# Performance work log

Hardware: AMD Instinct MI355X
Metric: run time of the kernel (lower is better)

The kernel has to match this reference:

```python
import jax, jax.numpy as jnp
import numpy as np

B, N, C, H, W = 4, 8, 256, 64, 64
K = 4          # BANK_SIZE
HID = 256      # HIDDEN_DIM
DT = 1.0
TEMP = 1.0     # RETRIEVAL_TEMPERATURE
NUM_ACTIONS = 5


def setup_inputs() -> dict:
    key = jax.random.key(0)
    ks = jax.random.split(key, 8)
    value = jax.random.normal(ks[0], (B, N, C, H, W), dtype=jnp.float32)
    mask = jax.random.uniform(ks[1], (B, N, H, W), dtype=jnp.float32)
    dict_keys = jax.random.normal(ks[2], (B, N, K, C), dtype=jnp.float32)
    dict_vel = jax.random.normal(ks[3], (B, N, K, C), dtype=jnp.float32) * 0.1
    dict_valid = jnp.ones((B, N, K), dtype=bool)
    din = 3 * C + K
    W1 = jax.random.normal(ks[4], (din, HID), dtype=jnp.float32) * 0.05
    b1 = jnp.zeros((HID,), dtype=jnp.float32)
    W2 = jax.random.normal(ks[5], (HID, NUM_ACTIONS), dtype=jnp.float32) * 0.05
    b2 = jnp.zeros((NUM_ACTIONS,), dtype=jnp.float32)
    gate = jnp.ones((1,), dtype=jnp.float32)
    return {"value": value, "mask": mask, "dict_keys": dict_keys, "dict_vel": dict_vel,
            "dict_valid": dict_valid, "W1": W1, "b1": b1, "W2": W2, "b2": b2, "gate": gate}


def _pool_state(value, mask):
    # masked mean pool over HxW (mask already at value resolution -> no interpolation branch)
    denom = mask.sum((-2, -1))                                           # [B,N]
    pooled = jnp.einsum('bnchw,bnhw->bnc', value, mask) / jnp.maximum(denom, 1e-6)[..., None]
    fallback = value.mean((-2, -1))                                      # [B,N,C]
    return jnp.where((denom > 1e-5)[..., None], pooled, fallback)


def _retrieve(z, keys, valid):
    dist = jnp.sum((z[:, :, None, :] - keys) ** 2, axis=-1)              # [B,N,K]
    logits = jnp.where(valid, -dist / TEMP, -1e30)
    w = jax.nn.softmax(logits, axis=-1)
    has = jnp.any(valid, axis=-1)                                        # [B,N]
    w = jnp.where(has[..., None], w, 0.0)
    nearest = jnp.argmin(jnp.where(valid, dist, jnp.inf), axis=-1)
    return w, nearest, has


def _forward(value, mask, dict_keys, dict_vel, dict_valid, W1, b1, W2, b2, gate):
    z = _pool_state(value, mask)                                         # [B,N,C]
    # first retrieval
    w0, n0, has0 = _retrieve(z, dict_keys, dict_valid)
    # branchless conditional spawn: write z into first free slot where no match
    need = ~has0                                                         # [B,N]
    slot = jnp.argmax(~dict_valid, axis=-1)                              # first invalid slot
    write = need[..., None] & (jnp.arange(K) == slot[..., None])         # [B,N,K]
    keys2 = jnp.where(write[..., None], z[:, :, None, :], dict_keys)
    vel2 = jnp.where(write[..., None], 0.0, dict_vel)
    valid2 = dict_valid | write
    # re-retrieve after (possible) spawn
    w, nearest, has = _retrieve(z, keys2, valid2)
    # ODE-style prediction: z_next = z + dt * sum_k w_k * vel_k
    vel_bar = jnp.einsum('bnk,bnkc->bnc', w, vel2)
    z_next = z + DT * vel_bar
    # Q maintainer: MLP over concat state, masked greedy action
    q_state = jnp.concatenate([z, z_next, z_next - z, w], axis=-1)       # [B,N,3C+K]
    h = jax.nn.relu(q_state @ W1 + b1)
    q = h @ W2 + b2                                                      # [B,N,5]
    bank_full = jnp.all(valid2, axis=-1)                                 # [B,N]
    action_mask = jnp.concatenate(
        [jnp.ones(q.shape[:-1] + (NUM_ACTIONS - 1,), bool), (~bank_full)[..., None]], axis=-1)
    q_values = jnp.where(action_mask, q, -1e9)
    actions = jnp.argmax(q_values, axis=-1)                              # [B,N]
    # Q-gated readout: broadcast delta over HxW
    delta = (z_next - z)[..., None, None]                                # [B,N,C,1,1]
    readout = value + gate[0] * delta
    wc = jnp.clip(w, 1e-8, None)
    entropy = -jnp.sum(wc * jnp.log(wc), axis=-1)                        # [B,N]
    hist = jnp.mean(jax.nn.one_hot(actions, NUM_ACTIONS, dtype=jnp.float32), axis=(0, 1))
    return readout, w, q_values, actions, entropy, hist


def reference(value, mask, dict_keys, dict_vel, dict_valid, W1, b1, W2, b2, gate):
    return _forward(value, mask, dict_keys, dict_vel, dict_valid, W1, b1, W2, b2, gate)
```

## Files before the change

kernel.cpp:

```cpp
#include <hip/hip_runtime.h>
#include <math.h>

#define B_ 4
#define N_ 8
#define C_ 256
#define H_ 64
#define Wd_ 64
#define K_ 4
#define HID_ 256
#define NA_ 5
#define HW_ (H_*Wd_)
#define DIN_ (3*C_+K_)
#define QS_STRIDE 800

#define READOUT_N (B_*N_*C_*HW_)
#define W_OFF    READOUT_N
#define Q_OFF    (W_OFF   + B_*N_*K_)
#define ACT_OFF  (Q_OFF   + B_*N_*NA_)
#define ENT_OFF  (ACT_OFF + B_*N_)
#define HIST_OFF (ENT_OFF + B_*N_)

__global__ __launch_bounds__(256) void pool_kernel(const float* __restrict__ value,
                                                   const float* __restrict__ mask,
                                                   float* __restrict__ z) {
    const int bnc = blockIdx.x;
    const int bn  = bnc >> 8;
    const int tid = threadIdx.x;
    const float4* vp = (const float4*)value + (size_t)bnc * (HW_/4);
    const float4* mp = (const float4*)mask  + (size_t)bn  * (HW_/4);
    float smv = 0.f, sv = 0.f, sm = 0.f;
    #pragma unroll
    for (int i = 0; i < (HW_/4)/256; ++i) {
        float4 v = vp[tid + i*256];
        float4 m = mp[tid + i*256];
        smv += v.x*m.x + v.y*m.y + v.z*m.z + v.w*m.w;
        sv  += v.x + v.y + v.z + v.w;
        sm  += m.x + m.y + m.z + m.w;
    }
    #pragma unroll
    for (int o = 32; o > 0; o >>= 1) {
        smv += __shfl_down(smv, o);
        sv  += __shfl_down(sv, o);
        sm  += __shfl_down(sm, o);
    }
    __shared__ float red[3][4];
    const int lane = tid & 63, wid = tid >> 6;
    if (lane == 0) { red[0][wid] = smv; red[1][wid] = sv; red[2][wid] = sm; }
    __syncthreads();
    if (tid == 0) {
        float t_smv = red[0][0]+red[0][1]+red[0][2]+red[0][3];
        float t_sv  = red[1][0]+red[1][1]+red[1][2]+red[1][3];
        float t_sm  = red[2][0]+red[2][1]+red[2][2]+red[2][3];
        float pooled = t_smv / fmaxf(t_sm, 1e-6f);
        float fb     = t_sv * (1.0f/HW_);
        z[bnc] = (t_sm > 1e-5f) ? pooled : fb;
    }
}

__global__ __launch_bounds__(256) void retrieve_kernel(
    const float* __restrict__ z,    const float* __restrict__ keys,
    const float* __restrict__ vel,  const int*   __restrict__ valid,
    float* __restrict__ qs_ws,      float* __restrict__ delta_ws,
    float* __restrict__ full_ws,    float* __restrict__ out)
{
    const int bn = blockIdx.x, tid = threadIdx.x;
    __shared__ float z_s[C_];
    __shared__ float key2[K_][C_];
    __shared__ float vel2[K_][C_];
    __shared__ float red[K_][4];
    __shared__ float w_s[K_];
    __shared__ int   wr_s[K_];
    __shared__ int   valid2_s[K_];

    z_s[tid] = z[bn*C_ + tid];
    if (tid == 0) {
        int v[K_]; bool anyv = false;
        for (int k = 0; k < K_; ++k) { v[k] = (valid[bn*K_ + k] != 0); anyv = anyv || v[k]; }
        int slot = 0;
        for (int k = K_-1; k >= 0; --k) if (!v[k]) slot = k;
        const bool need = !anyv;
        for (int k = 0; k < K_; ++k) {
            int wr = (need && k == slot) ? 1 : 0;
            wr_s[k] = wr;
            valid2_s[k] = v[k] | wr;
        }
    }
    __syncthreads();
    #pragma unroll
    for (int k = 0; k < K_; ++k) {
        key2[k][tid] = wr_s[k] ? z_s[tid] : keys[((size_t)bn*K_+k)*C_ + tid];
        vel2[k][tid] = wr_s[k] ? 0.f      : vel [((size_t)bn*K_+k)*C_ + tid];
    }
    __syncthreads();
    float part[K_];
    #pragma unroll
    for (int k = 0; k < K_; ++k) { float d = z_s[tid] - key2[k][tid]; part[k] = d*d; }
    #pragma unroll
    for (int o = 32; o > 0; o >>= 1) {
        #pragma unroll
        for (int k = 0; k < K_; ++k) part[k] += __shfl_down(part[k], o);
    }
    const int lane = tid & 63, wid = tid >> 6;
    if (lane == 0) { for (int k = 0; k < K_; ++k) red[k][wid] = part[k]; }
    __syncthreads();
    if (tid == 0) {
        float logit[K_], m = -3e38f;
        bool has = false;
        for (int k = 0; k < K_; ++k) {
            float dist = red[k][0]+red[k][1]+red[k][2]+red[k][3];
            bool vk = valid2_s[k] != 0;
            has = has || vk;
            logit[k] = vk ? -dist : -1e30f;
            m = fmaxf(m, logit[k]);
        }
        float s = 0.f, e[K_];
        for (int k = 0; k < K_; ++k) { e[k] = expf(logit[k] - m); s += e[k]; }
        for (int k = 0; k < K_; ++k) w_s[k] = has ? e[k]/s : 0.f;
        bool full = true;
        for (int k = 0; k < K_; ++k) full = full && (valid2_s[k] != 0);
        full_ws[bn] = full ? 1.f : 0.f;
        float ent = 0.f;
        for (int k = 0; k < K_; ++k) {
            out[W_OFF + bn*K_ + k] = w_s[k];
            float wc = fmaxf(w_s[k], 1e-8f);
            ent -= wc * logf(wc);
        }
        out[ENT_OFF + bn] = ent;
    }
    __syncthreads();
    float vb = 0.f;
    #pragma unroll
    for (int k = 0; k < K_; ++k) vb += w_s[k] * vel2[k][tid];
    const float zc = z_s[tid];
    delta_ws[bn*C_ + tid] = vb;
    float* qrow = qs_ws + bn*QS_STRIDE;
    qrow[tid]        = zc;
    qrow[C_   + tid] = zc + vb;
    qrow[2*C_ + tid] = vb;
    if (tid < K_) qrow[3*C_ + tid] = w_s[tid];
}

__global__ __launch_bounds__(256) void mlp1_kernel(const float* __restrict__ qs_ws,
                                                   const float* __restrict__ W1,
                                                   const float* __restrict__ b1,
                                                   float* __restrict__ h_ws) {
    const int blk = blockIdx.x;
    const int bn = blk >> 3, jb = blk & 7;
    const int tid = threadIdx.x;
    const int jg = tid & 31, ig = tid >> 5;
    const int j = jb*32 + jg;
    __shared__ float qs[DIN_];
    for (int i = tid; i < DIN_; i += 256) qs[i] = qs_ws[bn*QS_STRIDE + i];
    __syncthreads();
    float acc = 0.f;
    int i = ig;
    #pragma unroll 8
    for (int t = 0; t < 96; ++t, i += 8)
        acc = fmaf(qs[i], W1[(size_t)i*HID_ + j], acc);
    if (ig < 4)
        acc = fmaf(qs[768+ig], W1[(size_t)(768+ig)*HID_ + j], acc);
    __shared__ float part[8][33];
    part[ig][jg] = acc;
    __syncthreads();
    if (tid < 32) {
        float s = 0.f;
        #pragma unroll
        for (int g = 0; g < 8; ++g) s += part[g][tid];
        h_ws[bn*HID_ + jb*32 + tid] = fmaxf(s + b1[jb*32 + tid], 0.f);
    }
}

__global__ __launch_bounds__(256) void readout_kernel(const float* __restrict__ value,
                                                      const float* __restrict__ delta,
                                                      const float* __restrict__ gate,
                                                      const float* __restrict__ h_ws,
                                                      const float* __restrict__ W2,
                                                      const float* __restrict__ b2,
                                                      const float* __restrict__ full_ws,
                                                      float* __restrict__ out) {
    if (blockIdx.x == 0) {
        const int tid = threadIdx.x;
        __shared__ float qq[B_*N_][NA_];
        __shared__ int   act_s[B_*N_];
        if (tid < B_*N_*NA_) {
            const int bn = tid / NA_, a = tid % NA_;
            float acc = b2[a];
            const float* hp = h_ws + bn*HID_;
            #pragma unroll 8
            for (int jj = 0; jj < HID_; ++jj)
                acc = fmaf(hp[jj], W2[jj*NA_ + a], acc);
            const bool masked = (a == NA_-1) && (full_ws[bn] != 0.f);
            float qv = masked ? -1e9f : acc;
            out[Q_OFF + bn*NA_ + a] = qv;
            qq[bn][a] = qv;
        }
        __syncthreads();
        if (tid < B_*N_) {
            float best = -3.0e38f; int act = 0;
            #pragma unroll
            for (int a = 0; a < NA_; ++a) {
                float qv = qq[tid][a];
                if (qv > best) { best = qv; act = a; }
            }
            out[ACT_OFF + tid] = (float)act;
            act_s[tid] = act;
        }
        __syncthreads();
        if (tid < NA_) {
            float cnt = 0.f;
            for (int i = 0; i < B_*N_; ++i)
                if (act_s[i] == (int)tid) cnt += 1.f;
            out[HIST_OFF + tid] = cnt * (1.0f/(B_*N_));
        }
    }
    const float g = gate[0];
    const float4* vp = (const float4*)value;
    float4* op = (float4*)out;
    const int n4 = READOUT_N/4;
    for (int i = blockIdx.x*blockDim.x + threadIdx.x; i < n4; i += gridDim.x*blockDim.x) {
        float4 v = vp[i];
        float gd = g * delta[i >> 10];
        v.x += gd; v.y += gd; v.z += gd; v.w += gd;
        op[i] = v;
    }
}

extern "C" void kernel_launch(void* const* d_in, const int* in_sizes, int n_in,
                              void* d_out, int out_size, void* d_ws, size_t ws_size,
                              hipStream_t stream) {
    const float* value = (const float*)d_in[0];
    const float* mask  = (const float*)d_in[1];
    const float* keys  = (const float*)d_in[2];
    const float* vel   = (const float*)d_in[3];
    const int*   valid = (const int*)  d_in[4];
    const float* W1    = (const float*)d_in[5];
    const float* b1    = (const float*)d_in[6];
    const float* W2    = (const float*)d_in[7];
    const float* b2    = (const float*)d_in[8];
    const float* gate  = (const float*)d_in[9];
    float* out = (float*)d_out;

    float* z_ws     = (float*)d_ws;
    float* delta_ws = z_ws     + B_*N_*C_;
    float* qs_ws    = delta_ws + B_*N_*C_;
    float* h_ws     = qs_ws    + B_*N_*QS_STRIDE;
    float* full_ws  = h_ws     + B_*N_*HID_;

    pool_kernel<<<B_*N_*C_, 256, 0, stream>>>(value, mask, z_ws);
    retrieve_kernel<<<B_*N_, 256, 0, stream>>>(z_ws, keys, vel, valid, qs_ws, delta_ws, full_ws, out);
    mlp1_kernel<<<B_*N_*8, 256, 0, stream>>>(qs_ws, W1, b1, h_ws);
    readout_kernel<<<2048, 256, 0, stream>>>(value, delta_ws, gate, h_ws, W2, b2, full_ws, out);
}
```

Before: 84.71 us.

## Fuse retrieval into MLP1 kernel and restructure readout with nontemporal per-channel blocks

```diff
diff --git a/kernel.cpp b/kernel.cpp
--- a/kernel.cpp
+++ b/kernel.cpp
@@ -11,7 +11,8 @@
 #define NA_ 5
 #define HW_ (H_*Wd_)
 #define DIN_ (3*C_+K_)
-#define QS_STRIDE 800
+
+typedef float vfloat4 __attribute__((ext_vector_type(4)));
 
 #define READOUT_N (B_*N_*C_*HW_)
 #define W_OFF    READOUT_N
@@ -57,22 +58,23 @@
     }
 }
 
-__global__ __launch_bounds__(256) void retrieve_kernel(
+__global__ __launch_bounds__(256) void brain_kernel(
     const float* __restrict__ z,    const float* __restrict__ keys,
     const float* __restrict__ vel,  const int*   __restrict__ valid,
-    float* __restrict__ qs_ws,      float* __restrict__ delta_ws,
+    const float* __restrict__ W1,   const float* __restrict__ b1,
+    float* __restrict__ delta_ws,   float* __restrict__ h_ws,
     float* __restrict__ full_ws,    float* __restrict__ out)
 {
-    const int bn = blockIdx.x, tid = threadIdx.x;
-    __shared__ float z_s[C_];
-    __shared__ float key2[K_][C_];
-    __shared__ float vel2[K_][C_];
+    const int blk = blockIdx.x;
+    const int bn = blk >> 3, jb = blk & 7;
+    const int tid = threadIdx.x;
+    __shared__ float qs[DIN_];
     __shared__ float red[K_][4];
     __shared__ float w_s[K_];
     __shared__ int   wr_s[K_];
     __shared__ int   valid2_s[K_];
 
-    z_s[tid] = z[bn*C_ + tid];
+    const float zc = z[bn*C_ + tid];
     if (tid == 0) {
         int v[K_]; bool anyv = false;
         for (int k = 0; k < K_; ++k) { v[k] = (valid[bn*K_ + k] != 0); anyv = anyv || v[k]; }
@@ -86,15 +88,14 @@
         }
     }
     __syncthreads();
+    float vv[K_], part[K_];
     #pragma unroll
     for (int k = 0; k < K_; ++k) {
-        key2[k][tid] = wr_s[k] ? z_s[tid] : keys[((size_t)bn*K_+k)*C_ + tid];
-        vel2[k][tid] = wr_s[k] ? 0.f      : vel [((size_t)bn*K_+k)*C_ + tid];
-    }
-    __syncthreads();
-    float part[K_];
-    #pragma unroll
-    for (int k = 0; k < K_; ++k) { float d = z_s[tid] - key2[k][tid]; part[k] = d*d; }
+        const float kv = wr_s[k] ? zc : keys[((size_t)bn*K_+k)*C_ + tid];
+        vv[k] = wr_s[k] ? 0.f : vel[((size_t)bn*K_+k)*C_ + tid];
+        const float d = zc - kv;
+        part[k] = d*d;
+    }
     #pragma unroll
     for (int o = 32; o > 0; o >>= 1) {
         #pragma unroll
@@ -116,42 +117,31 @@
         float s = 0.f, e[K_];
         for (int k = 0; k < K_; ++k) { e[k] = expf(logit[k] - m); s += e[k]; }
         for (int k = 0; k < K_; ++k) w_s[k] = has ? e[k]/s : 0.f;
-        bool full = true;
-        for (int k = 0; k < K_; ++k) full = full && (valid2_s[k] != 0);
-        full_ws[bn] = full ? 1.f : 0.f;
-        float ent = 0.f;
-        for (int k = 0; k < K_; ++k) {
-            out[W_OFF + bn*K_ + k] = w_s[k];
-            float wc = fmaxf(w_s[k], 1e-8f);
-            ent -= wc * logf(wc);
-        }
-        out[ENT_OFF + bn] = ent;
+        if (jb == 0) {
+            bool full = true;
+            for (int k = 0; k < K_; ++k) full = full && (valid2_s[k] != 0);
+            full_ws[bn] = full ? 1.f : 0.f;
+            float ent = 0.f;
+            for (int k = 0; k < K_; ++k) {
+                out[W_OFF + bn*K_ + k] = w_s[k];
+                float wc = fmaxf(w_s[k], 1e-8f);
+                ent -= wc * logf(wc);
+            }
+            out[ENT_OFF + bn] = ent;
+        }
     }
     __syncthreads();
     float vb = 0.f;
     #pragma unroll
-    for (int k = 0; k < K_; ++k) vb += w_s[k] * vel2[k][tid];
-    const float zc = z_s[tid];
-    delta_ws[bn*C_ + tid] = vb;
-    float* qrow = qs_ws + bn*QS_STRIDE;
-    qrow[tid]        = zc;
-    qrow[C_   + tid] = zc + vb;
-    qrow[2*C_ + tid] = vb;
-    if (tid < K_) qrow[3*C_ + tid] = w_s[tid];
-}
-
-__global__ __launch_bounds__(256) void mlp1_kernel(const float* __restrict__ qs_ws,
-                                                   const float* __restrict__ W1,
-                                                   const float* __restrict__ b1,
-                                                   float* __restrict__ h_ws) {
-    const int blk = blockIdx.x;
-    const int bn = blk >> 3, jb = blk & 7;
-    const int tid = threadIdx.x;
+    for (int k = 0; k < K_; ++k) vb += w_s[k] * vv[k];
+    qs[tid]        = zc;
+    qs[C_   + tid] = zc + vb;
+    qs[2*C_ + tid] = vb;
+    if (tid < K_) qs[3*C_ + tid] = w_s[tid];
+    if (jb == 0) delta_ws[bn*C_ + tid] = vb;
+    __syncthreads();
     const int jg = tid & 31, ig = tid >> 5;
     const int j = jb*32 + jg;
-    __shared__ float qs[DIN_];
-    for (int i = tid; i < DIN_; i += 256) qs[i] = qs_ws[bn*QS_STRIDE + i];
-    __syncthreads();
     float acc = 0.f;
     int i = ig;
     #pragma unroll 8
@@ -159,13 +149,13 @@
         acc = fmaf(qs[i], W1[(size_t)i*HID_ + j], acc);
     if (ig < 4)
         acc = fmaf(qs[768+ig], W1[(size_t)(768+ig)*HID_ + j], acc);
-    __shared__ float part[8][33];
-    part[ig][jg] = acc;
+    __shared__ float part_s[8][33];
+    part_s[ig][jg] = acc;
     __syncthreads();
     if (tid < 32) {
         float s = 0.f;
         #pragma unroll
-        for (int g = 0; g < 8; ++g) s += part[g][tid];
+        for (int g = 0; g < 8; ++g) s += part_s[g][tid];
         h_ws[bn*HID_ + jb*32 + tid] = fmaxf(s + b1[jb*32 + tid], 0.f);
     }
 }
@@ -178,8 +168,9 @@
                                                       const float* __restrict__ b2,
                                                       const float* __restrict__ full_ws,
                                                       float* __restrict__ out) {
-    if (blockIdx.x == 0) {
-        const int tid = threadIdx.x;
+    const int bnc = blockIdx.x;
+    const int tid = threadIdx.x;
+    if (bnc == 0) {
         __shared__ float qq[B_*N_][NA_];
         __shared__ int   act_s[B_*N_];
         if (tid < B_*N_*NA_) {
@@ -213,15 +204,15 @@
             out[HIST_OFF + tid] = cnt * (1.0f/(B_*N_));
         }
     }
-    const float g = gate[0];
-    const float4* vp = (const float4*)value;
-    float4* op = (float4*)out;
-    const int n4 = READOUT_N/4;
-    for (int i = blockIdx.x*blockDim.x + threadIdx.x; i < n4; i += gridDim.x*blockDim.x) {
-        float4 v = vp[i];
-        float gd = g * delta[i >> 10];
-        v.x += gd; v.y += gd; v.z += gd; v.w += gd;
-        op[i] = v;
+    const float gd = gate[0] * delta[bnc];
+    const vfloat4* vp = (const vfloat4*)value + (size_t)bnc * (HW_/4);
+    vfloat4*       op = (vfloat4*)out         + (size_t)bnc * (HW_/4);
+    #pragma unroll
+    for (int t = 0; t < (HW_/4)/256; ++t) {
+        const int idx = tid + t*256;
+        vfloat4 v = __builtin_nontemporal_load(&vp[idx]);
+        v += gd;
+        __builtin_nontemporal_store(v, &op[idx]);
     }
 }
 
@@ -242,12 +233,10 @@
 
     float* z_ws     = (float*)d_ws;
     float* delta_ws = z_ws     + B_*N_*C_;
-    float* qs_ws    = delta_ws + B_*N_*C_;
-    float* h_ws     = qs_ws    + B_*N_*QS_STRIDE;
+    float* h_ws     = delta_ws + B_*N_*C_;
     float* full_ws  = h_ws     + B_*N_*HID_;
 
     pool_kernel<<<B_*N_*C_, 256, 0, stream>>>(value, mask, z_ws);
-    retrieve_kernel<<<B_*N_, 256, 0, stream>>>(z_ws, keys, vel, valid, qs_ws, delta_ws, full_ws, out);
-    mlp1_kernel<<<B_*N_*8, 256, 0, stream>>>(qs_ws, W1, b1, h_ws);
-    readout_kernel<<<2048, 256, 0, stream>>>(value, delta_ws, gate, h_ws, W2, b2, full_ws, out);
-}
+    brain_kernel<<<B_*N_*8, 256, 0, stream>>>(z_ws, keys, vel, valid, W1, b1, delta_ws, h_ws, full_ws, out);
+    readout_kernel<<<B_*N_*C_, 256, 0, stream>>>(value, delta_ws, gate, h_ws, W2, b2, full_ws, out);
+}
```

Result: faster. 72.67 us (-14.2%).
